# Kernel tuning notes

Hardware: AMD Instinct MI355X
Metric: run time of the kernel (lower is better)

## Reference

```python
import jax, jax.numpy as jnp
import numpy as np
import math

THETA = 10000.0

def _rope(x, pos):
    # x: [B, H, S, Dh], pos: [S]
    d = x.shape[-1]
    inv_freq = 1.0 / (THETA ** (jnp.arange(0, d, 2, dtype=jnp.float32) / d))  # [Dh/2]
    ang = pos.astype(jnp.float32)[:, None] * inv_freq[None, :]                # [S, Dh/2]
    cos, sin = jnp.cos(ang), jnp.sin(ang)
    x1, x2 = x[..., 0::2], x[..., 1::2]
    r1 = x1 * cos - x2 * sin
    r2 = x1 * sin + x2 * cos
    return jnp.stack([r1, r2], axis=-1).reshape(x.shape)

def setup_inputs() -> dict:
    key = jax.random.key(0)
    ks = jax.random.split(key, 5)
    B, S, D = 2, 1024, 2048
    Dkv = 512
    scale = 1.0 / math.sqrt(D)
    return {
        "X": jax.random.normal(ks[0], (B, S, D), dtype=jnp.float32),
        "token_positions": jnp.arange(S, dtype=jnp.int32),
        "q_w": jax.random.normal(ks[1], (D, D), dtype=jnp.float32) * scale,
        "k_w": jax.random.normal(ks[2], (Dkv, D), dtype=jnp.float32) * scale,
        "v_w": jax.random.normal(ks[3], (Dkv, D), dtype=jnp.float32) * scale,
        "o_w": jax.random.normal(ks[4], (D, D), dtype=jnp.float32) * scale,
    }

def reference(X, token_positions, q_w, k_w, v_w, o_w):
    B, S, D = X.shape
    H, Hkv = 32, 8
    Dh = D // H
    G = H // Hkv  # query heads per KV head

    Q = (X @ q_w.T).reshape(B, S, H, Dh).transpose(0, 2, 1, 3)      # [B,H,S,Dh]
    K = (X @ k_w.T).reshape(B, S, Hkv, Dh).transpose(0, 2, 1, 3)    # [B,Hkv,S,Dh]
    V = (X @ v_w.T).reshape(B, S, Hkv, Dh).transpose(0, 2, 1, 3)    # [B,Hkv,S,Dh]

    Q = _rope(Q, token_positions)
    K = _rope(K, token_positions)

    # group query heads: [B, Hkv, G, S, Dh]
    Qg = Q.reshape(B, Hkv, G, S, Dh)
    scores = jnp.einsum('bkgqd,bkld->bkgql', Qg, K) / math.sqrt(Dh)  # [B,Hkv,G,S,S]
    causal = jnp.tril(jnp.ones((S, S), dtype=bool))
    scores = jnp.where(causal, scores, -jnp.inf)
    probs = jax.nn.softmax(scores, axis=-1)
    attn = jnp.einsum('bkgql,bkld->bkgqd', probs, V)                 # [B,Hkv,G,S,Dh]

    attn = attn.reshape(B, H, S, Dh).transpose(0, 2, 1, 3).reshape(B, S, D)
    return attn @ o_w.T
```

## Files before the change

kernel.cpp:

```cpp
#include <hip/hip_runtime.h>

typedef _Float16 f16;
typedef _Float16 half8 __attribute__((ext_vector_type(8), may_alias));
typedef _Float16 half4 __attribute__((ext_vector_type(4), may_alias));
typedef float f32x4 __attribute__((ext_vector_type(4), may_alias));

#define ROPE_KF -0.41524101186092027f

__device__ __forceinline__ void gload_lds16(const f16* g, f16* lds) {
  __builtin_amdgcn_global_load_lds(
      (const __attribute__((address_space(1))) void*)g,
      (__attribute__((address_space(3))) void*)lds, 16, 0, 0);
}

__device__ __forceinline__ half8 rope8(half8 v, float posf, int i0, float scale) {
  half8 r;
#pragma unroll
  for (int p = 0; p < 4; ++p) {
    const float ang = posf * exp2f(ROPE_KF * (float)(i0 + p));
    float s, c;
    sincosf(ang, &s, &c);
    const float x1 = (float)v[2 * p], x2 = (float)v[2 * p + 1];
    r[2 * p]     = (f16)((x1 * c - x2 * s) * scale);
    r[2 * p + 1] = (f16)((x1 * s + x2 * c) * scale);
  }
  return r;
}

__global__ __launch_bounds__(256) void cvt_all(const float* __restrict__ s0, f16* __restrict__ d0, int n0,
                                               const float* __restrict__ s1, f16* __restrict__ d1, int n1,
                                               const float* __restrict__ s2, f16* __restrict__ d2, int n2,
                                               const float* __restrict__ s3, f16* __restrict__ d3, int n3,
                                               const float* __restrict__ s4, f16* __restrict__ d4, int n4) {
  const int step = gridDim.x * blockDim.x * 4;
  const int base = (blockIdx.x * blockDim.x + threadIdx.x) * 4;
  auto go = [&](const float* s, f16* d, int n) {
    for (int i = base; i < n; i += step) {
      float4 v = *(const float4*)(s + i);
      half4 h;
      h[0] = (f16)v.x; h[1] = (f16)v.y; h[2] = (f16)v.z; h[3] = (f16)v.w;
      *(half4*)(d + i) = h;
    }
  };
  go(s0, d0, n0); go(s1, d1, n1); go(s2, d2, n2); go(s3, d3, n3); go(s4, d4, n4);
}

template <int OUT_F32>
__global__ __launch_bounds__(256) void gemm_bt(const f16* __restrict__ A,
                                               const f16* __restrict__ B,
                                               void* __restrict__ Cv,
                                               int M, int N, int K) {
  __shared__ alignas(16) f16 As[2][64][32];
  __shared__ alignas(16) f16 Bs[2][128][32];
  const int tid = threadIdx.x;
  const int w = tid >> 6, l = tid & 63;
  const int m0 = blockIdx.y << 6, n0 = blockIdx.x << 7;
  const int fr = l & 15;
  const int fkz = (((l >> 4) ^ ((fr >> 1) & 3)) << 3);
  const int srow = l >> 2;
  const int scol = (((l & 3) ^ ((l >> 3) & 3)) << 3);

  const f16* ga  = A + (size_t)(m0 + w * 16 + srow) * K + scol;
  const f16* gb0 = B + (size_t)(n0 + w * 16 + srow) * K + scol;
  const f16* gb1 = B + (size_t)(n0 + 64 + w * 16 + srow) * K + scol;

  auto stage = [&](int buf, int k0) {
    gload_lds16(ga + k0, &As[buf][w * 16][0]);
    gload_lds16(gb0 + k0, &Bs[buf][w * 16][0]);
    gload_lds16(gb1 + k0, &Bs[buf][64 + w * 16][0]);
  };

  f32x4 acc[4][2] = {};

  stage(0, 0);
  __syncthreads();
  const int nk = K >> 5;
  for (int t = 0; t < nk; ++t) {
    const int buf = t & 1;
    if (t + 1 < nk) stage(buf ^ 1, (t + 1) << 5);
    half8 af[4], bf[2];
#pragma unroll
    for (int i = 0; i < 4; ++i) af[i] = *(const half8*)&As[buf][i * 16 + fr][fkz];
#pragma unroll
    for (int j = 0; j < 2; ++j) bf[j] = *(const half8*)&Bs[buf][w * 32 + j * 16 + fr][fkz];
#pragma unroll
    for (int i = 0; i < 4; ++i)
#pragma unroll
      for (int j = 0; j < 2; ++j)
        acc[i][j] = __builtin_amdgcn_mfma_f32_16x16x32_f16(af[i], bf[j], acc[i][j], 0, 0, 0);
    __syncthreads();
  }

  const int orow = (l >> 4) << 2;
#pragma unroll
  for (int i = 0; i < 4; ++i) {
#pragma unroll
    for (int j = 0; j < 2; ++j) {
      const int col = n0 + w * 32 + j * 16 + fr;
#pragma unroll
      for (int r = 0; r < 4; ++r) {
        const size_t idx = (size_t)(m0 + i * 16 + orow + r) * N + col;
        if (OUT_F32) ((float*)Cv)[idx] = acc[i][j][r];
        else ((f16*)Cv)[idx] = (f16)acc[i][j][r];
      }
    }
  }
}

__global__ __launch_bounds__(256) void repack_kv(const f16* __restrict__ QKV,
                                                 const int* __restrict__ pos,
                                                 f16* __restrict__ Kp,
                                                 f16* __restrict__ Vt) {
  const int kt = blockIdx.x, kvh = blockIdx.y, b = blockIdx.z;
  const int tid = threadIdx.x;
  __shared__ f16 vs[64][72];
  const size_t tile = ((size_t)((b * 8 + kvh) * 16 + kt)) * 4096;
  const f16* kbase = QKV + 2048 + kvh * 64;
  const f16* vbase = QKV + 2560 + kvh * 64;
#pragma unroll
  for (int p = 0; p < 2; ++p) {
    const int c = tid + p * 256;
    const int row = c >> 3, slot = c & 7;
    const size_t grow = (size_t)(b * 1024 + kt * 64 + row) * 3072;
    half8 kk = *(const half8*)(kbase + grow + slot * 8);
    kk = rope8(kk, (float)pos[kt * 64 + row], slot << 2, 1.0f);
    *(half8*)(Kp + tile + row * 64 + ((slot ^ (row & 7)) << 3)) = kk;
    *(half8*)&vs[row][slot * 8] = *(const half8*)(vbase + grow + slot * 8);
  }
  __syncthreads();
#pragma unroll
  for (int p = 0; p < 2; ++p) {
    const int c = tid + p * 256;
    const int d = c >> 3, oct = c & 7;
    half8 vv;
#pragma unroll
    for (int m = 0; m < 8; ++m) vv[m] = vs[oct * 8 + m][d];
    *(half8*)(Vt + tile + d * 64 + ((oct ^ (d & 7)) << 3)) = vv;
  }
}

__global__ __launch_bounds__(256) void attn_fwd(const f16* __restrict__ QKV,
                                                const f16* __restrict__ Kp,
                                                const f16* __restrict__ Vt,
                                                const int* __restrict__ pos,
                                                f16* __restrict__ O) {
  const int flat = blockIdx.x + (blockIdx.y << 3) + (blockIdx.z << 8);
  const int rmid = ((flat & 7) << 6) + (flat >> 3);
  const int pr = rmid & 7, h = (rmid >> 3) & 31, b = rmid >> 8;
  const int kvh = h >> 2;
  const int tid = threadIdx.x, w = tid >> 6, l = tid & 63;
  const int fr = l & 15, g = l >> 4;
  const int orow = g << 2;
  const int qtA = pr, qtB = 15 - pr;

  __shared__ alignas(16) char KsB[2][8192];
  __shared__ alignas(16) char VtB[2][8192];
  __shared__ alignas(16) f16 Ps[4][16][72];

  auto KS = [&](int buf, int row, int slot) -> f16* {
    return (f16*)(KsB[buf] + row * 128 + ((slot ^ (row & 7)) << 4));
  };
  auto VT = [&](int buf, int d, int oct) -> f16* {
    return (f16*)(VtB[buf] + d * 128 + ((oct ^ (d & 7)) << 4));
  };

  const int sA = qtA * 64 + w * 16 + fr, sB = qtB * 64 + w * 16 + fr;
  const float pA = (float)pos[sA], pB = (float)pos[sB];
  const size_t qoff = (size_t)(b * 1024 + w * 16 + fr) * 3072 + h * 64 + (g << 3);
  const f16* qA = QKV + qoff + (size_t)qtA * 64 * 3072;
  const f16* qB = QKV + qoff + (size_t)qtB * 64 * 3072;
  const half8 aA0 = rope8(*(const half8*)qA, pA, g << 2, 0.125f);
  const half8 aA1 = rope8(*(const half8*)(qA + 32), pA, 16 + (g << 2), 0.125f);
  const half8 aB0 = rope8(*(const half8*)qB, pB, g << 2, 0.125f);
  const half8 aB1 = rope8(*(const half8*)(qB + 32), pB, 16 + (g << 2), 0.125f);

  float rmA[4], rlA[4], rmB[4], rlB[4];
  f32x4 oA[4] = {}, oB[4] = {};
#pragma unroll
  for (int r = 0; r < 4; ++r) { rmA[r] = rmB[r] = -3.0e38f; rlA[r] = rlB[r] = 0.f; }

  const size_t tbase = ((size_t)((b * 8 + kvh) * 16)) * 4096;
  const f16* kp0 = Kp + tbase + w * 1024 + (l << 3);
  const f16* vp0 = Vt + tbase + w * 1024 + (l << 3);
  auto stage = [&](int buf, int kt) {
    const f16* kp = kp0 + (size_t)kt * 4096;
    const f16* vp = vp0 + (size_t)kt * 4096;
    f16* kl = (f16*)(KsB[buf] + w * 2048);
    f16* vl = (f16*)(VtB[buf] + w * 2048);
    gload_lds16(kp, kl);
    gload_lds16(kp + 512, kl + 512);
    gload_lds16(vp, vl);
    gload_lds16(vp + 512, vl + 512);
  };

  auto compute = [&](int buf, const half8& a0, const half8& a1, float* rm, float* rl,
                     f32x4* o, int qt, int kt) {
    f32x4 s4[4] = {};
#pragma unroll
    for (int j = 0; j < 4; ++j) {
      const half8 bk0 = *(const half8*)KS(buf, j * 16 + fr, g);
      const half8 bk1 = *(const half8*)KS(buf, j * 16 + fr, 4 + g);
      s4[j] = __builtin_amdgcn_mfma_f32_16x16x32_f16(a0, bk0, s4[j], 0, 0, 0);
      s4[j] = __builtin_amdgcn_mfma_f32_16x16x32_f16(a1, bk1, s4[j], 0, 0, 0);
    }
    if (kt == qt) {
      const int qrow0 = qt * 64 + w * 16 + orow;
#pragma unroll
      for (int j = 0; j < 4; ++j) {
        const int col = kt * 64 + j * 16 + fr;
#pragma unroll
        for (int r = 0; r < 4; ++r)
          if (col > qrow0 + r) s4[j][r] = -1.0e30f;
      }
    }
#pragma unroll
    for (int r = 0; r < 4; ++r) {
      float mx = fmaxf(fmaxf(s4[0][r], s4[1][r]), fmaxf(s4[2][r], s4[3][r]));
#pragma unroll
      for (int off = 8; off >= 1; off >>= 1) mx = fmaxf(mx, __shfl_xor(mx, off));
      const float mn = fmaxf(rm[r], mx);
      const float sf = __expf(rm[r] - mn);
      rl[r] *= sf;
      o[0][r] *= sf; o[1][r] *= sf; o[2][r] *= sf; o[3][r] *= sf;
      rm[r] = mn;
    }
    float ps[4] = {0.f, 0.f, 0.f, 0.f};
#pragma unroll
    for (int j = 0; j < 4; ++j)
#pragma unroll
      for (int r = 0; r < 4; ++r) {
        const float p = __expf(s4[j][r] - rm[r]);
        ps[r] += p;
        Ps[w][orow + r][j * 16 + fr] = (f16)p;
      }
#pragma unroll
    for (int r = 0; r < 4; ++r) {
      float t = ps[r];
#pragma unroll
      for (int off = 8; off >= 1; off >>= 1) t += __shfl_xor(t, off);
      rl[r] += t;
    }
#pragma unroll
    for (int kv2 = 0; kv2 < 2; ++kv2) {
      const half8 ap = *(const half8*)&Ps[w][fr][kv2 * 32 + (g << 3)];
#pragma unroll
      for (int j = 0; j < 4; ++j) {
        const half8 bv = *(const half8*)VT(buf, j * 16 + fr, kv2 * 4 + g);
        o[j] = __builtin_amdgcn_mfma_f32_16x16x32_f16(ap, bv, o[j], 0, 0, 0);
      }
    }
  };

  stage(0, 0);
  __syncthreads();
  for (int kt = 0; kt <= qtB; ++kt) {
    const int buf = kt & 1;
    if (kt < qtB) stage(buf ^ 1, kt + 1);
    if (kt <= qtA) compute(buf, aA0, aA1, rmA, rlA, oA, qtA, kt);
    compute(buf, aB0, aB1, rmB, rlB, oB, qtB, kt);
    __syncthreads();
  }

#pragma unroll
  for (int j = 0; j < 4; ++j)
#pragma unroll
    for (int r = 0; r < 4; ++r) {
      const int rowA = qtA * 64 + w * 16 + orow + r;
      const int rowB = qtB * 64 + w * 16 + orow + r;
      const int col = h * 64 + j * 16 + fr;
      O[(size_t)(b * 1024 + rowA) * 2048 + col] = (f16)(oA[j][r] / rlA[r]);
      O[(size_t)(b * 1024 + rowB) * 2048 + col] = (f16)(oB[j][r] / rlB[r]);
    }
}

extern "C" void kernel_launch(void* const* d_in, const int* in_sizes, int n_in,
                              void* d_out, int out_size, void* d_ws, size_t ws_size,
                              hipStream_t stream) {
  const float* X = (const float*)d_in[0];
  const int* tokpos = (const int*)d_in[1];
  const float* qw = (const float*)d_in[2];
  const float* kw = (const float*)d_in[3];
  const float* vw = (const float*)d_in[4];
  const float* ow = (const float*)d_in[5];

  constexpr int B = 2, S = 1024, D = 2048, DKV = 512, H = 32;
  constexpr int M = B * S;
  constexpr int NQKV = D + 2 * DKV;

  char* ws = (char*)d_ws;
  f16* Xh   = (f16*)(ws);
  f16* QKVW = (f16*)(ws + (8u << 20));
  f16* owh  = (f16*)(ws + (20u << 20));
  f16* QKVc = (f16*)(ws + (28u << 20));
  f16* Ah   = (f16*)(ws + (40u << 20));
  f16* Kp   = (f16*)(ws);
  f16* Vt   = (f16*)(ws + (2u << 20));

  cvt_all<<<2048, 256, 0, stream>>>(X, Xh, M * D,
                                    qw, QKVW, D * D,
                                    kw, QKVW + (size_t)D * D, DKV * D,
                                    vw, QKVW + (size_t)(D + DKV) * D, DKV * D,
                                    ow, owh, D * D);

  gemm_bt<0><<<dim3(NQKV / 128, M / 64), 256, 0, stream>>>(Xh, QKVW, QKVc, M, NQKV, D);

  repack_kv<<<dim3(16, 8, 2), 256, 0, stream>>>(QKVc, tokpos, Kp, Vt);

  attn_fwd<<<dim3(8, H, B), 256, 0, stream>>>(QKVc, Kp, Vt, tokpos, Ah);

  gemm_bt<1><<<dim3(D / 128, M / 64), 256, 0, stream>>>(Ah, owh, d_out, M, D, D);
}
```

Baseline: 140.2 us.

## Deepen GEMM and attention load pipelines with vmcnt waits and larger QKV tile

Both the GEMM and the attention loop now issue the next two stages of async global-to-LDS loads up front. They use explicit s_waitcnt vmcnt counts plus raw s_barrier in place of __syncthreads, so the following tile's loads stay in flight during compute. The QKV projection GEMM also moves to a 128x128 block tile with a 2x2 wave layout for more operand reuse per LDS load, and launch bounds now request 2 blocks per CU. The risks are correctness of the hand-counted vmcnt values and higher register pressure from the larger accumulator tile.

```diff
diff --git a/kernel.cpp b/kernel.cpp
--- a/kernel.cpp
+++ b/kernel.cpp
@@ -11,6 +11,13 @@
   __builtin_amdgcn_global_load_lds(
       (const __attribute__((address_space(1))) void*)g,
       (__attribute__((address_space(3))) void*)lds, 16, 0, 0);
+}
+
+template <int N>
+__device__ __forceinline__ void waitcnt_vm() {
+  if constexpr (N == 0) asm volatile("s_waitcnt vmcnt(0)" ::: "memory");
+  else if constexpr (N == 3) asm volatile("s_waitcnt vmcnt(3)" ::: "memory");
+  else if constexpr (N == 4) asm volatile("s_waitcnt vmcnt(4)" ::: "memory");
 }
 
 __device__ __forceinline__ half8 rope8(half8 v, float posf, int i0, float scale) {
@@ -45,61 +52,79 @@
   go(s0, d0, n0); go(s1, d1, n1); go(s2, d2, n2); go(s3, d3, n3); go(s4, d4, n4);
 }
 
-template <int OUT_F32>
-__global__ __launch_bounds__(256) void gemm_bt(const f16* __restrict__ A,
-                                               const f16* __restrict__ B,
-                                               void* __restrict__ Cv,
-                                               int M, int N, int K) {
-  __shared__ alignas(16) f16 As[2][64][32];
+template <int OUT_F32, int BM>
+__global__ __launch_bounds__(256, 2) void gemm_bt(const f16* __restrict__ A,
+                                                  const f16* __restrict__ B,
+                                                  void* __restrict__ Cv,
+                                                  int M, int N, int K) {
+  constexpr int NJ = (BM == 128) ? 4 : 2;
+  constexpr int ACH = BM / 64;
+  constexpr int LPS = ACH + 2;
+
+  __shared__ alignas(16) f16 As[2][BM][32];
   __shared__ alignas(16) f16 Bs[2][128][32];
   const int tid = threadIdx.x;
   const int w = tid >> 6, l = tid & 63;
-  const int m0 = blockIdx.y << 6, n0 = blockIdx.x << 7;
+  const int m0 = blockIdx.y * BM, n0 = blockIdx.x << 7;
   const int fr = l & 15;
   const int fkz = (((l >> 4) ^ ((fr >> 1) & 3)) << 3);
+  const int wr = (BM == 128) ? ((w >> 1) << 6) : 0;
+  const int wc = (BM == 128) ? ((w & 1) << 6) : (w << 5);
   const int srow = l >> 2;
   const int scol = (((l & 3) ^ ((l >> 3) & 3)) << 3);
 
-  const f16* ga  = A + (size_t)(m0 + w * 16 + srow) * K + scol;
-  const f16* gb0 = B + (size_t)(n0 + w * 16 + srow) * K + scol;
-  const f16* gb1 = B + (size_t)(n0 + 64 + w * 16 + srow) * K + scol;
-
-  auto stage = [&](int buf, int k0) {
-    gload_lds16(ga + k0, &As[buf][w * 16][0]);
-    gload_lds16(gb0 + k0, &Bs[buf][w * 16][0]);
-    gload_lds16(gb1 + k0, &Bs[buf][64 + w * 16][0]);
-  };
-
-  f32x4 acc[4][2] = {};
-
+  const f16* ga = A + (size_t)(m0 + srow) * K + scol;
+  const f16* gb = B + (size_t)(n0 + srow) * K + scol;
+
+  auto stage = [&](int buf, int t) {
+    const int k0 = t << 5;
+#pragma unroll
+    for (int c = 0; c < ACH; ++c) {
+      const int rb = (w * ACH + c) << 4;
+      gload_lds16(ga + (size_t)rb * K + k0, &As[buf][rb][0]);
+    }
+#pragma unroll
+    for (int c = 0; c < 2; ++c) {
+      const int rb = (w * 2 + c) << 4;
+      gload_lds16(gb + (size_t)rb * K + k0, &Bs[buf][rb][0]);
+    }
+  };
+
+  f32x4 acc[4][NJ] = {};
+
+  const int nk = K >> 5;
   stage(0, 0);
-  __syncthreads();
-  const int nk = K >> 5;
+  stage(1, 1);
   for (int t = 0; t < nk; ++t) {
     const int buf = t & 1;
-    if (t + 1 < nk) stage(buf ^ 1, (t + 1) << 5);
-    half8 af[4], bf[2];
-#pragma unroll
-    for (int i = 0; i < 4; ++i) af[i] = *(const half8*)&As[buf][i * 16 + fr][fkz];
-#pragma unroll
-    for (int j = 0; j < 2; ++j) bf[j] = *(const half8*)&Bs[buf][w * 32 + j * 16 + fr][fkz];
+    if (t + 1 < nk) waitcnt_vm<LPS>();
+    else waitcnt_vm<0>();
+    __builtin_amdgcn_s_barrier();
+    __builtin_amdgcn_sched_barrier(0);
+    half8 af[4], bf[NJ];
+#pragma unroll
+    for (int i = 0; i < 4; ++i) af[i] = *(const half8*)&As[buf][wr + i * 16 + fr][fkz];
+#pragma unroll
+    for (int j = 0; j < NJ; ++j) bf[j] = *(const half8*)&Bs[buf][wc + j * 16 + fr][fkz];
 #pragma unroll
     for (int i = 0; i < 4; ++i)
 #pragma unroll
-      for (int j = 0; j < 2; ++j)
+      for (int j = 0; j < NJ; ++j)
         acc[i][j] = __builtin_amdgcn_mfma_f32_16x16x32_f16(af[i], bf[j], acc[i][j], 0, 0, 0);
-    __syncthreads();
+    __builtin_amdgcn_sched_barrier(0);
+    __builtin_amdgcn_s_barrier();
+    if (t + 2 < nk) stage(buf, t + 2);
   }
 
   const int orow = (l >> 4) << 2;
 #pragma unroll
   for (int i = 0; i < 4; ++i) {
 #pragma unroll
-    for (int j = 0; j < 2; ++j) {
-      const int col = n0 + w * 32 + j * 16 + fr;
+    for (int j = 0; j < NJ; ++j) {
+      const int col = n0 + wc + j * 16 + fr;
 #pragma unroll
       for (int r = 0; r < 4; ++r) {
-        const size_t idx = (size_t)(m0 + i * 16 + orow + r) * N + col;
+        const size_t idx = (size_t)(m0 + wr + i * 16 + orow + r) * N + col;
         if (OUT_F32) ((float*)Cv)[idx] = acc[i][j][r];
         else ((f16*)Cv)[idx] = (f16)acc[i][j][r];
       }
@@ -252,13 +277,18 @@
   };
 
   stage(0, 0);
-  __syncthreads();
+  stage(1, 1);
   for (int kt = 0; kt <= qtB; ++kt) {
     const int buf = kt & 1;
-    if (kt < qtB) stage(buf ^ 1, kt + 1);
+    if (kt < qtB) waitcnt_vm<4>();
+    else waitcnt_vm<0>();
+    __builtin_amdgcn_s_barrier();
+    __builtin_amdgcn_sched_barrier(0);
     if (kt <= qtA) compute(buf, aA0, aA1, rmA, rlA, oA, qtA, kt);
     compute(buf, aB0, aB1, rmB, rlB, oB, qtB, kt);
-    __syncthreads();
+    __builtin_amdgcn_sched_barrier(0);
+    __builtin_amdgcn_s_barrier();
+    if (kt + 2 <= qtB) stage(buf, kt + 2);
   }
 
 #pragma unroll
@@ -302,11 +332,11 @@
                                     vw, QKVW + (size_t)(D + DKV) * D, DKV * D,
                                     ow, owh, D * D);
 
-  gemm_bt<0><<<dim3(NQKV / 128, M / 64), 256, 0, stream>>>(Xh, QKVW, QKVc, M, NQKV, D);
+  gemm_bt<0, 128><<<dim3(NQKV / 128, M / 128), 256, 0, stream>>>(Xh, QKVW, QKVc, M, NQKV, D);
 
   repack_kv<<<dim3(16, 8, 2), 256, 0, stream>>>(QKVc, tokpos, Kp, Vt);
 
   attn_fwd<<<dim3(8, H, B), 256, 0, stream>>>(QKVc, Kp, Vt, tokpos, Ah);
 
-  gemm_bt<1><<<dim3(D / 128, M / 64), 256, 0, stream>>>(Ah, owh, d_out, M, D, D);
-}
+  gemm_bt<1, 64><<<dim3(D / 128, M / 64), 256, 0, stream>>>(Ah, owh, d_out, M, D, D);
+}
```

New measurement: 137.5 us. No clear change (-1.9%).
